# Kernel optimization log

Hardware: AMD Instinct MI355X
Metric: run time of the kernel (lower is better)

## Reference

```python
import jax, jax.numpy as jnp
import numpy as np

N_NODES = 50000
N_EDGES = 600000
H_DIM = 128
BN_EPS = 1e-5


def setup_inputs() -> dict:
    key = jax.random.key(0)
    k1, k2, k3, k4 = jax.random.split(key, 4)
    ent_emb = jax.random.normal(k1, (N_NODES, H_DIM), dtype=jnp.float32)
    # xavier_normal_ init for the 128x128 weight
    std = float(np.sqrt(2.0 / (H_DIM + H_DIM)))
    neigh_w = jax.random.normal(k2, (H_DIM, H_DIM), dtype=jnp.float32) * std
    gamma = jnp.ones((H_DIM,), dtype=jnp.float32)
    beta = jnp.zeros((H_DIM,), dtype=jnp.float32)
    src = jax.random.randint(k3, (N_EDGES,), 0, N_NODES, dtype=jnp.int32)
    dst = jax.random.randint(k4, (N_EDGES,), 0, N_NODES, dtype=jnp.int32)
    return {"ent_emb": ent_emb, "neigh_w": neigh_w, "gamma": gamma,
            "beta": beta, "src": src, "dst": dst}


def reference(ent_emb, neigh_w, gamma, beta, src, dst):
    # Edge dot-product scores: u_dot_v('emb','emb')  -> [E]
    e_src = ent_emb[src]                      # [E, H]
    e_dst = ent_emb[dst]                      # [E, H]
    scores = jnp.sum(e_src * e_dst, axis=-1)  # [E]

    # edge_softmax: softmax over incoming edges of each destination node
    seg_max = jax.ops.segment_max(scores, dst, num_segments=N_NODES)
    seg_max = jnp.where(jnp.isfinite(seg_max), seg_max, 0.0)  # nodes w/o edges
    e = jnp.exp(scores - seg_max[dst])                         # [E]
    seg_sum = jax.ops.segment_sum(e, dst, num_segments=N_NODES)
    norm = e / seg_sum[dst]                                    # [E]

    # update_all(u_mul_e, sum): weighted gather-sum aggregation
    msg = e_src * norm[:, None]                                # [E, H]
    neigh = jax.ops.segment_sum(msg, dst, num_segments=N_NODES)  # [N, H]

    # matmul + BatchNorm1d (training-mode batch stats) + tanh
    h = neigh @ neigh_w                                        # [N, H]
    mean = jnp.mean(h, axis=0)
    var = jnp.var(h, axis=0)  # biased, matches torch BN normalization
    h = (h - mean) * jax.lax.rsqrt(var + BN_EPS) * gamma + beta
    return jnp.tanh(h)
```

## Files before the change

kernel.cpp:

```cpp
#include <hip/hip_runtime.h>
#include <math.h>

#define N_NODES 50000
#define N_EDGES 600000
#define H 128
#define BN_EPS 1e-5f
#define MAXDEG 48

__global__ void k_scatter(const int* __restrict__ src, const int* __restrict__ dst,
                          int* __restrict__ cnt, int* __restrict__ slots) {
    int i = blockIdx.x * blockDim.x + threadIdx.x;
    if (i < N_EDGES) {
        int d = dst[i];
        int pos = atomicAdd(cnt + d, 1);
        if (pos < MAXDEG) slots[d * MAXDEG + pos] = src[i];
    }
}

#define F4SCALE(a, s) { (a).x *= (s); (a).y *= (s); (a).z *= (s); (a).w *= (s); }
#define F4FMA(a, e, v) { (a).x += (e)*(v).x; (a).y += (e)*(v).y; (a).z += (e)*(v).z; (a).w += (e)*(v).w; }
#define F4SHFLADD(a, msk) { (a).x += __shfl_xor((a).x, msk, 64); (a).y += __shfl_xor((a).y, msk, 64); \
                            (a).z += __shfl_xor((a).z, msk, 64); (a).w += __shfl_xor((a).w, msk, 64); }

__global__ __launch_bounds__(256) void k_fused(const float* __restrict__ emb,
                                               const int* __restrict__ cnt,
                                               const int* __restrict__ slots,
                                               float* __restrict__ neigh) {
    int wid = (blockIdx.x * blockDim.x + threadIdx.x) >> 6;
    int lane = threadIdx.x & 63;
    if (wid >= N_NODES) return;
    int g = lane >> 3;
    int l = lane & 7;

    int deg = min(cnt[wid], MAXDEG);
    int sid = slots[wid * MAXDEG + min(lane, MAXDEG - 1)];

    const float4* rd = (const float4*)(emb + (size_t)wid * H) + l * 4;
    float4 b0 = rd[0], b1 = rd[1], b2 = rd[2], b3 = rd[3];

    float m = -INFINITY, ssum = 0.0f;
    float4 acc0 = {0,0,0,0}, acc1 = {0,0,0,0}, acc2 = {0,0,0,0}, acc3 = {0,0,0,0};

    for (int cb = 0; cb < deg; cb += 8) {
        int e = cb + g;
        bool valid = e < deg;
        int s = __shfl(sid, valid ? e : 0, 64);
        const float4* rs = (const float4*)(emb + (size_t)s * H) + l * 4;
        float4 a0 = rs[0], a1 = rs[1], a2 = rs[2], a3 = rs[3];

        float v = a0.x*b0.x + a0.y*b0.y + a0.z*b0.z + a0.w*b0.w
                + a1.x*b1.x + a1.y*b1.y + a1.z*b1.z + a1.w*b1.w
                + a2.x*b2.x + a2.y*b2.y + a2.z*b2.z + a2.w*b2.w
                + a3.x*b3.x + a3.y*b3.y + a3.z*b3.z + a3.w*b3.w;
        v += __shfl_xor(v, 1, 64);
        v += __shfl_xor(v, 2, 64);
        v += __shfl_xor(v, 4, 64);
        if (!valid) v = -INFINITY;

        float cmax = v;
        cmax = fmaxf(cmax, __shfl_xor(cmax, 8, 64));
        cmax = fmaxf(cmax, __shfl_xor(cmax, 16, 64));
        cmax = fmaxf(cmax, __shfl_xor(cmax, 32, 64));
        float mnew = fmaxf(m, cmax);
        float scale = __expf(m - mnew);
        ssum *= scale;
        F4SCALE(acc0, scale); F4SCALE(acc1, scale);
        F4SCALE(acc2, scale); F4SCALE(acc3, scale);
        m = mnew;

        float ev = __expf(v - m);
        ssum += ev;
        F4FMA(acc0, ev, a0); F4FMA(acc1, ev, a1);
        F4FMA(acc2, ev, a2); F4FMA(acc3, ev, a3);
    }

    ssum += __shfl_xor(ssum, 8, 64);
    ssum += __shfl_xor(ssum, 16, 64);
    ssum += __shfl_xor(ssum, 32, 64);
    F4SHFLADD(acc0, 8);  F4SHFLADD(acc1, 8);  F4SHFLADD(acc2, 8);  F4SHFLADD(acc3, 8);
    F4SHFLADD(acc0, 16); F4SHFLADD(acc1, 16); F4SHFLADD(acc2, 16); F4SHFLADD(acc3, 16);
    F4SHFLADD(acc0, 32); F4SHFLADD(acc1, 32); F4SHFLADD(acc2, 32); F4SHFLADD(acc3, 32);

    float inv = (deg > 0) ? 1.0f / ssum : 0.0f;
    if (g == 0) {
        float4* po = (float4*)(neigh + (size_t)wid * H) + l * 4;
        F4SCALE(acc0, inv); F4SCALE(acc1, inv); F4SCALE(acc2, inv); F4SCALE(acc3, inv);
        po[0] = acc0; po[1] = acc1; po[2] = acc2; po[3] = acc3;
    }
}

#define MM_ROWS 128
#define MM_COLS 64
__global__ __launch_bounds__(256, 4) void k_matmul(const float* __restrict__ neigh,
                                                   const float* __restrict__ W,
                                                   float* __restrict__ hout,
                                                   float* __restrict__ stats) {
    __shared__ float Wl[H * MM_COLS];
    __shared__ float Sl[16 * MM_COLS];
    __shared__ float Ql[16 * MM_COLS];
    int t = threadIdx.x;
    int bc = blockIdx.x & 1;
    int br = blockIdx.x >> 1;
    int c0 = bc * MM_COLS;
    int n0 = br * MM_ROWS;
    int cg = t & 15, rg = t >> 4;
    int j0 = cg * 4;
    int r0 = n0 + rg * 8;

    for (int idx = t; idx < H * 16; idx += 256) {
        int k = idx >> 4, c4 = idx & 15;
        *(float4*)&Wl[k * MM_COLS + c4 * 4] =
            *((const float4*)(W + (size_t)k * H + c0) + c4);
    }

    const float* pr[8];
    bool valid[8];
#pragma unroll
    for (int i = 0; i < 8; ++i) {
        int n = r0 + i;
        valid[i] = (n < N_NODES);
        pr[i] = neigh + (size_t)(valid[i] ? n : 0) * H;
    }

    __syncthreads();

    float acc[8][4] = {};
    for (int k0 = 0; k0 < H; k0 += 4) {
        float4 rv[8];
#pragma unroll
        for (int i = 0; i < 8; ++i) rv[i] = *(const float4*)(pr[i] + k0);
        float4 wv[4];
#pragma unroll
        for (int kk = 0; kk < 4; ++kk) wv[kk] = *(const float4*)&Wl[(k0 + kk) * MM_COLS + j0];
#pragma unroll
        for (int kk = 0; kk < 4; ++kk) {
#pragma unroll
            for (int i = 0; i < 8; ++i) {
                float rk = ((const float*)&rv[i])[kk];
                acc[i][0] += rk * wv[kk].x;
                acc[i][1] += rk * wv[kk].y;
                acc[i][2] += rk * wv[kk].z;
                acc[i][3] += rk * wv[kk].w;
            }
        }
    }

#pragma unroll
    for (int i = 0; i < 8; ++i) {
        if (valid[i]) {
            float4 o = make_float4(acc[i][0], acc[i][1], acc[i][2], acc[i][3]);
            *(float4*)(hout + (size_t)(r0 + i) * H + c0 + j0) = o;
        }
    }

#pragma unroll
    for (int c = 0; c < 4; ++c) {
        float s = 0.0f, q = 0.0f;
#pragma unroll
        for (int i = 0; i < 8; ++i) {
            if (valid[i]) { s += acc[i][c]; q += acc[i][c] * acc[i][c]; }
        }
        Sl[rg * MM_COLS + j0 + c] = s;
        Ql[rg * MM_COLS + j0 + c] = q;
    }
    __syncthreads();
    if (t < MM_COLS) {
        float s = 0.0f;
#pragma unroll
        for (int r = 0; r < 16; ++r) s += Sl[r * MM_COLS + t];
        atomicAdd(stats + c0 + t, s);
    } else if (t < 2 * MM_COLS) {
        int j = t - MM_COLS;
        float q = 0.0f;
#pragma unroll
        for (int r = 0; r < 16; ++r) q += Ql[r * MM_COLS + j];
        atomicAdd(stats + 128 + c0 + j, q);
    }
}

__device__ __forceinline__ float tanh_fast(float x) {
    float e = __expf(2.0f * x);
    return 1.0f - 2.0f / (e + 1.0f);
}

__global__ __launch_bounds__(256) void k_apply(float* __restrict__ h,
                                               const float* __restrict__ stats,
                                               const float* __restrict__ gamma,
                                               const float* __restrict__ beta) {
    __shared__ float sc[128], sh[128];
    int t = threadIdx.x;
    if (t < 128) {
        float mean = stats[t] * (1.0f / N_NODES);
        float var = stats[128 + t] * (1.0f / N_NODES) - mean * mean;
        var = fmaxf(var, 0.0f);
        float s = gamma[t] * rsqrtf(var + BN_EPS);
        sc[t] = s;
        sh[t] = beta[t] - mean * s;
    }
    __syncthreads();
    int i = blockIdx.x * 256 + t;
    if (i < N_NODES * H / 4) {
        float4 v = ((const float4*)h)[i];
        int jb = (i & 31) * 4;
        v.x = tanh_fast(v.x * sc[jb]     + sh[jb]);
        v.y = tanh_fast(v.y * sc[jb + 1] + sh[jb + 1]);
        v.z = tanh_fast(v.z * sc[jb + 2] + sh[jb + 2]);
        v.w = tanh_fast(v.w * sc[jb + 3] + sh[jb + 3]);
        ((float4*)h)[i] = v;
    }
}

extern "C" void kernel_launch(void* const* d_in, const int* in_sizes, int n_in,
                              void* d_out, int out_size, void* d_ws, size_t ws_size,
                              hipStream_t stream) {
    const float* emb   = (const float*)d_in[0];
    const float* W     = (const float*)d_in[1];
    const float* gamma = (const float*)d_in[2];
    const float* beta  = (const float*)d_in[3];
    const int*   src   = (const int*)d_in[4];
    const int*   dst   = (const int*)d_in[5];
    float* out = (float*)d_out;

    int*   cnt   = (int*)d_ws;
    float* stats = (float*)(cnt + N_NODES);
    int*   slots = (int*)(stats + 256);
    float* neigh = (float*)(slots + (size_t)N_NODES * MAXDEG);

    hipMemsetAsync(cnt, 0, (N_NODES + 256) * sizeof(int), stream);
    k_scatter<<<(N_EDGES + 255) / 256, 256, 0, stream>>>(src, dst, cnt, slots);
    k_fused<<<(N_NODES * 64 + 255) / 256, 256, 0, stream>>>(emb, cnt, slots, neigh);
    k_matmul<<<((N_NODES + MM_ROWS - 1) / MM_ROWS) * 2, 256, 0, stream>>>(neigh, W, out, stats);
    k_apply<<<(N_NODES * H / 4 + 255) / 256, 256, 0, stream>>>(out, stats, gamma, beta);
}
```

Before: 216.9 us.

## Fuse all stages into one persistent cooperative kernel with grid syncs

Replaces the memset plus four kernel launches with a single cooperative persistent kernel that runs scatter, attention aggregation, matmul with BN stats, and BN+tanh apply, separated by grid-wide barriers. The aim is to remove launch overhead and inter-kernel gaps. In exchange the grid is capped at 4 blocks per CU across 256 CUs, so work is done in grid-stride loops with less parallelism per phase. Grid syncs and thread fences add their own cost. The old multi-kernel path is kept as a fallback if the cooperative launch fails.

```diff
diff --git a/kernel.cpp b/kernel.cpp
--- a/kernel.cpp
+++ b/kernel.cpp
@@ -1,11 +1,228 @@
 #include <hip/hip_runtime.h>
+#include <hip/hip_cooperative_groups.h>
 #include <math.h>
+
+namespace cg = cooperative_groups;
 
 #define N_NODES 50000
 #define N_EDGES 600000
 #define H 128
 #define BN_EPS 1e-5f
 #define MAXDEG 48
+#define NT 256
+#define MM_ROWS 128
+#define MM_COLS 64
+#define ROW_TILES ((N_NODES + MM_ROWS - 1) / MM_ROWS)
+#define N_TILES (ROW_TILES * 2)
+
+#define F4SCALE(a, s) { (a).x *= (s); (a).y *= (s); (a).z *= (s); (a).w *= (s); }
+#define F4FMA(a, e, v) { (a).x += (e)*(v).x; (a).y += (e)*(v).y; (a).z += (e)*(v).z; (a).w += (e)*(v).w; }
+#define F4SHFLADD(a, msk) { (a).x += __shfl_xor((a).x, msk, 64); (a).y += __shfl_xor((a).y, msk, 64); \
+                            (a).z += __shfl_xor((a).z, msk, 64); (a).w += __shfl_xor((a).w, msk, 64); }
+
+__device__ __forceinline__ float tanh_fast(float x) {
+    float e = __expf(2.0f * x);
+    return 1.0f - 2.0f / (e + 1.0f);
+}
+
+__global__ __launch_bounds__(256, 4) void k_mega(
+    const float* __restrict__ emb, const float* __restrict__ W,
+    const float* __restrict__ gamma, const float* __restrict__ beta,
+    const int* __restrict__ src, const int* __restrict__ dst,
+    int* __restrict__ cnt, int* __restrict__ slots,
+    float* __restrict__ neigh, float* __restrict__ stats,
+    float* __restrict__ out)
+{
+    cg::grid_group gg = cg::this_grid();
+    __shared__ float Wl[H * MM_COLS];
+    __shared__ float Sl[16 * MM_COLS];
+    __shared__ float Ql[16 * MM_COLS];
+
+    int t = threadIdx.x;
+    int b = blockIdx.x;
+    int nb = gridDim.x;
+    int gtid = b * NT + t;
+    int gsz = nb * NT;
+
+    for (int i = gtid; i < N_NODES; i += gsz) cnt[i] = 0;
+    if (gtid < 256) stats[gtid] = 0.0f;
+    gg.sync();
+
+    for (int i = gtid; i < N_EDGES; i += gsz) {
+        int d = dst[i];
+        int pos = atomicAdd(cnt + d, 1);
+        if (pos < MAXDEG) slots[d * MAXDEG + pos] = src[i];
+    }
+    __threadfence();
+    gg.sync();
+
+    {
+        int lane = t & 63;
+        int g = lane >> 3;
+        int l = lane & 7;
+        for (int wid = gtid >> 6; wid < N_NODES; wid += gsz >> 6) {
+            int deg = min(cnt[wid], MAXDEG);
+            int sid = slots[wid * MAXDEG + min(lane, MAXDEG - 1)];
+
+            const float4* rd = (const float4*)(emb + (size_t)wid * H) + l * 4;
+            float4 b0 = rd[0], b1 = rd[1], b2 = rd[2], b3 = rd[3];
+
+            float m = -INFINITY, ssum = 0.0f;
+            float4 acc0 = {0,0,0,0}, acc1 = {0,0,0,0}, acc2 = {0,0,0,0}, acc3 = {0,0,0,0};
+
+            for (int cb = 0; cb < deg; cb += 8) {
+                int e = cb + g;
+                bool ok = e < deg;
+                int s = __shfl(sid, ok ? e : 0, 64);
+                const float4* rs = (const float4*)(emb + (size_t)s * H) + l * 4;
+                float4 a0 = rs[0], a1 = rs[1], a2 = rs[2], a3 = rs[3];
+
+                float v = a0.x*b0.x + a0.y*b0.y + a0.z*b0.z + a0.w*b0.w
+                        + a1.x*b1.x + a1.y*b1.y + a1.z*b1.z + a1.w*b1.w
+                        + a2.x*b2.x + a2.y*b2.y + a2.z*b2.z + a2.w*b2.w
+                        + a3.x*b3.x + a3.y*b3.y + a3.z*b3.z + a3.w*b3.w;
+                v += __shfl_xor(v, 1, 64);
+                v += __shfl_xor(v, 2, 64);
+                v += __shfl_xor(v, 4, 64);
+                if (!ok) v = -INFINITY;
+
+                float cmax = v;
+                cmax = fmaxf(cmax, __shfl_xor(cmax, 8, 64));
+                cmax = fmaxf(cmax, __shfl_xor(cmax, 16, 64));
+                cmax = fmaxf(cmax, __shfl_xor(cmax, 32, 64));
+                float mnew = fmaxf(m, cmax);
+                float scale = __expf(m - mnew);
+                ssum *= scale;
+                F4SCALE(acc0, scale); F4SCALE(acc1, scale);
+                F4SCALE(acc2, scale); F4SCALE(acc3, scale);
+                m = mnew;
+
+                float ev = __expf(v - m);
+                ssum += ev;
+                F4FMA(acc0, ev, a0); F4FMA(acc1, ev, a1);
+                F4FMA(acc2, ev, a2); F4FMA(acc3, ev, a3);
+            }
+
+            ssum += __shfl_xor(ssum, 8, 64);
+            ssum += __shfl_xor(ssum, 16, 64);
+            ssum += __shfl_xor(ssum, 32, 64);
+            F4SHFLADD(acc0, 8);  F4SHFLADD(acc1, 8);  F4SHFLADD(acc2, 8);  F4SHFLADD(acc3, 8);
+            F4SHFLADD(acc0, 16); F4SHFLADD(acc1, 16); F4SHFLADD(acc2, 16); F4SHFLADD(acc3, 16);
+            F4SHFLADD(acc0, 32); F4SHFLADD(acc1, 32); F4SHFLADD(acc2, 32); F4SHFLADD(acc3, 32);
+
+            float inv = (deg > 0) ? 1.0f / ssum : 0.0f;
+            if (g == 0) {
+                float4* po = (float4*)(neigh + (size_t)wid * H) + l * 4;
+                F4SCALE(acc0, inv); F4SCALE(acc1, inv); F4SCALE(acc2, inv); F4SCALE(acc3, inv);
+                po[0] = acc0; po[1] = acc1; po[2] = acc2; po[3] = acc3;
+            }
+        }
+    }
+    __threadfence();
+    gg.sync();
+
+    {
+        int cgc = t & 15, rg = t >> 4;
+        int j0 = cgc * 4;
+        for (int tile = b; tile < N_TILES; tile += nb) {
+            int c0 = (tile & 1) * MM_COLS;
+            int r0 = (tile >> 1) * MM_ROWS + rg * 8;
+
+            __syncthreads();
+            for (int idx = t; idx < H * 16; idx += NT) {
+                int k = idx >> 4, c4 = idx & 15;
+                *(float4*)&Wl[k * MM_COLS + c4 * 4] =
+                    *((const float4*)(W + (size_t)k * H + c0) + c4);
+            }
+            const float* pr[8];
+            bool valid[8];
+#pragma unroll
+            for (int i = 0; i < 8; ++i) {
+                int n = r0 + i;
+                valid[i] = (n < N_NODES);
+                pr[i] = neigh + (size_t)(valid[i] ? n : 0) * H;
+            }
+            __syncthreads();
+
+            float acc[8][4] = {};
+            for (int k0 = 0; k0 < H; k0 += 4) {
+                float4 rv[8];
+#pragma unroll
+                for (int i = 0; i < 8; ++i) rv[i] = *(const float4*)(pr[i] + k0);
+                float4 wv[4];
+#pragma unroll
+                for (int kk = 0; kk < 4; ++kk) wv[kk] = *(const float4*)&Wl[(k0 + kk) * MM_COLS + j0];
+#pragma unroll
+                for (int kk = 0; kk < 4; ++kk) {
+#pragma unroll
+                    for (int i = 0; i < 8; ++i) {
+                        float rk = ((const float*)&rv[i])[kk];
+                        acc[i][0] += rk * wv[kk].x;
+                        acc[i][1] += rk * wv[kk].y;
+                        acc[i][2] += rk * wv[kk].z;
+                        acc[i][3] += rk * wv[kk].w;
+                    }
+                }
+            }
+
+#pragma unroll
+            for (int i = 0; i < 8; ++i) {
+                if (valid[i]) {
+                    float4 o = make_float4(acc[i][0], acc[i][1], acc[i][2], acc[i][3]);
+                    *(float4*)(out + (size_t)(r0 + i) * H + c0 + j0) = o;
+                }
+            }
+
+#pragma unroll
+            for (int c = 0; c < 4; ++c) {
+                float s = 0.0f, q = 0.0f;
+#pragma unroll
+                for (int i = 0; i < 8; ++i) {
+                    if (valid[i]) { s += acc[i][c]; q += acc[i][c] * acc[i][c]; }
+                }
+                Sl[rg * MM_COLS + j0 + c] = s;
+                Ql[rg * MM_COLS + j0 + c] = q;
+            }
+            __syncthreads();
+            if (t < MM_COLS) {
+                float s = 0.0f;
+#pragma unroll
+                for (int r = 0; r < 16; ++r) s += Sl[r * MM_COLS + t];
+                atomicAdd(stats + c0 + t, s);
+            } else if (t < 2 * MM_COLS) {
+                int j = t - MM_COLS;
+                float q = 0.0f;
+#pragma unroll
+                for (int r = 0; r < 16; ++r) q += Ql[r * MM_COLS + j];
+                atomicAdd(stats + 128 + c0 + j, q);
+            }
+        }
+    }
+    __threadfence();
+    gg.sync();
+
+    {
+        float* scA = Sl;
+        float* shA = Ql;
+        if (t < 128) {
+            float mean = stats[t] * (1.0f / N_NODES);
+            float var = fmaxf(stats[128 + t] * (1.0f / N_NODES) - mean * mean, 0.0f);
+            float s = gamma[t] * rsqrtf(var + BN_EPS);
+            scA[t] = s;
+            shA[t] = beta[t] - mean * s;
+        }
+        __syncthreads();
+        for (int i = gtid; i < N_NODES * H / 4; i += gsz) {
+            float4 v = ((const float4*)out)[i];
+            int jb = (i & 31) * 4;
+            v.x = tanh_fast(v.x * scA[jb]     + shA[jb]);
+            v.y = tanh_fast(v.y * scA[jb + 1] + shA[jb + 1]);
+            v.z = tanh_fast(v.z * scA[jb + 2] + shA[jb + 2]);
+            v.w = tanh_fast(v.w * scA[jb + 3] + shA[jb + 3]);
+            ((float4*)out)[i] = v;
+        }
+    }
+}
 
 __global__ void k_scatter(const int* __restrict__ src, const int* __restrict__ dst,
                           int* __restrict__ cnt, int* __restrict__ slots) {
@@ -16,11 +233,6 @@
         if (pos < MAXDEG) slots[d * MAXDEG + pos] = src[i];
     }
 }
-
-#define F4SCALE(a, s) { (a).x *= (s); (a).y *= (s); (a).z *= (s); (a).w *= (s); }
-#define F4FMA(a, e, v) { (a).x += (e)*(v).x; (a).y += (e)*(v).y; (a).z += (e)*(v).z; (a).w += (e)*(v).w; }
-#define F4SHFLADD(a, msk) { (a).x += __shfl_xor((a).x, msk, 64); (a).y += __shfl_xor((a).y, msk, 64); \
-                            (a).z += __shfl_xor((a).z, msk, 64); (a).w += __shfl_xor((a).w, msk, 64); }
 
 __global__ __launch_bounds__(256) void k_fused(const float* __restrict__ emb,
                                                const int* __restrict__ cnt,
@@ -43,8 +255,8 @@
 
     for (int cb = 0; cb < deg; cb += 8) {
         int e = cb + g;
-        bool valid = e < deg;
-        int s = __shfl(sid, valid ? e : 0, 64);
+        bool ok = e < deg;
+        int s = __shfl(sid, ok ? e : 0, 64);
         const float4* rs = (const float4*)(emb + (size_t)s * H) + l * 4;
         float4 a0 = rs[0], a1 = rs[1], a2 = rs[2], a3 = rs[3];
 
@@ -55,7 +267,7 @@
         v += __shfl_xor(v, 1, 64);
         v += __shfl_xor(v, 2, 64);
         v += __shfl_xor(v, 4, 64);
-        if (!valid) v = -INFINITY;
+        if (!ok) v = -INFINITY;
 
         float cmax = v;
         cmax = fmaxf(cmax, __shfl_xor(cmax, 8, 64));
@@ -89,8 +301,6 @@
     }
 }
 
-#define MM_ROWS 128
-#define MM_COLS 64
 __global__ __launch_bounds__(256, 4) void k_matmul(const float* __restrict__ neigh,
                                                    const float* __restrict__ W,
                                                    float* __restrict__ hout,
@@ -103,8 +313,8 @@
     int br = blockIdx.x >> 1;
     int c0 = bc * MM_COLS;
     int n0 = br * MM_ROWS;
-    int cg = t & 15, rg = t >> 4;
-    int j0 = cg * 4;
+    int cg2 = t & 15, rg = t >> 4;
+    int j0 = cg2 * 4;
     int r0 = n0 + rg * 8;
 
     for (int idx = t; idx < H * 16; idx += 256) {
@@ -112,7 +322,6 @@
         *(float4*)&Wl[k * MM_COLS + c4 * 4] =
             *((const float4*)(W + (size_t)k * H + c0) + c4);
     }
-
     const float* pr[8];
     bool valid[8];
 #pragma unroll
@@ -121,7 +330,6 @@
         valid[i] = (n < N_NODES);
         pr[i] = neigh + (size_t)(valid[i] ? n : 0) * H;
     }
-
     __syncthreads();
 
     float acc[8][4] = {};
@@ -176,11 +384,6 @@
         for (int r = 0; r < 16; ++r) q += Ql[r * MM_COLS + j];
         atomicAdd(stats + 128 + c0 + j, q);
     }
-}
-
-__device__ __forceinline__ float tanh_fast(float x) {
-    float e = __expf(2.0f * x);
-    return 1.0f - 2.0f / (e + 1.0f);
 }
 
 __global__ __launch_bounds__(256) void k_apply(float* __restrict__ h,
@@ -191,8 +394,7 @@
     int t = threadIdx.x;
     if (t < 128) {
         float mean = stats[t] * (1.0f / N_NODES);
-        float var = stats[128 + t] * (1.0f / N_NODES) - mean * mean;
-        var = fmaxf(var, 0.0f);
+        float var = fmaxf(stats[128 + t] * (1.0f / N_NODES) - mean * mean, 0.0f);
         float s = gamma[t] * rsqrtf(var + BN_EPS);
         sc[t] = s;
         sh[t] = beta[t] - mean * s;
@@ -226,9 +428,23 @@
     int*   slots = (int*)(stats + 256);
     float* neigh = (float*)(slots + (size_t)N_NODES * MAXDEG);
 
-    hipMemsetAsync(cnt, 0, (N_NODES + 256) * sizeof(int), stream);
-    k_scatter<<<(N_EDGES + 255) / 256, 256, 0, stream>>>(src, dst, cnt, slots);
-    k_fused<<<(N_NODES * 64 + 255) / 256, 256, 0, stream>>>(emb, cnt, slots, neigh);
-    k_matmul<<<((N_NODES + MM_ROWS - 1) / MM_ROWS) * 2, 256, 0, stream>>>(neigh, W, out, stats);
-    k_apply<<<(N_NODES * H / 4 + 255) / 256, 256, 0, stream>>>(out, stats, gamma, beta);
-}
+    int nb = 0;
+    hipError_t qerr = hipOccupancyMaxActiveBlocksPerMultiprocessor(&nb, k_mega, NT, 0);
+    hipError_t lerr = hipErrorUnknown;
+    if (qerr == hipSuccess && nb > 0) {
+        int bpc = nb < 4 ? nb : 4;
+        int grid = bpc * 256;
+        void* args[] = { (void*)&emb, (void*)&W, (void*)&gamma, (void*)&beta,
+                         (void*)&src, (void*)&dst, (void*)&cnt, (void*)&slots,
+                         (void*)&neigh, (void*)&stats, (void*)&out };
+        lerr = hipLaunchCooperativeKernel(reinterpret_cast<const void*>(k_mega),
+                                          dim3(grid), dim3(NT), args, 0, stream);
+    }
+    if (lerr != hipSuccess) {
+        hipMemsetAsync(cnt, 0, (N_NODES + 256) * sizeof(int), stream);
+        k_scatter<<<(N_EDGES + 255) / 256, 256, 0, stream>>>(src, dst, cnt, slots);
+        k_fused<<<(N_NODES * 64 + 255) / 256, 256, 0, stream>>>(emb, cnt, slots, neigh);
+        k_matmul<<<N_TILES, 256, 0, stream>>>(neigh, W, out, stats);
+        k_apply<<<(N_NODES * H / 4 + 255) / 256, 256, 0, stream>>>(out, stats, gamma, beta);
+    }
+}
```

Result: slower. 648.2 us (+198.8%).
